# Kernel optimization log

Measured on AMD Instinct MI355X. Metric: run time of the kernel, lower is better.

## Reference

```python
import jax, jax.numpy as jnp
import numpy as np

B, S, D = 2, 2048, 1024
H = 16
DH = D // H  # 64
LN_EPS = 1e-3  # keras LayerNormalization default epsilon


def _layer_norm(x, gamma, beta):
    mu = jnp.mean(x, axis=-1, keepdims=True)
    var = jnp.mean(jnp.square(x - mu), axis=-1, keepdims=True)
    return (x - mu) * jax.lax.rsqrt(var + LN_EPS) * gamma + beta


def setup_inputs() -> dict:
    key = jax.random.key(0)
    ks = jax.random.split(key, 7)
    he = lambda k, fi, fo: jax.random.normal(k, (fi, fo), jnp.float32) * np.sqrt(2.0 / fi)
    return {
        "query": jax.random.normal(ks[0], (B, S, D), jnp.float32),
        "Wq": he(ks[1], D, D),
        "Wk": he(ks[2], D, D),
        "Wv": he(ks[3], D, D),
        "W1": he(ks[4], D, D),
        "W2": he(ks[5], D, D),
        "W3": he(ks[6], D, D),
        "gamma": jnp.ones((D,), jnp.float32),
        "beta": jnp.zeros((D,), jnp.float32),
    }


def reference(query, Wq, Wk, Wv, W1, W2, W3, gamma, beta):
    # self-attention: key = value = query; do_residual = True
    def split_heads(t):  # [B,S,D] -> [B,H,S,DH]
        return t.reshape(B, S, H, DH).transpose(0, 2, 1, 3)

    q = split_heads(query @ Wq)
    k = split_heads(query @ Wk)
    v = split_heads(query @ Wv)

    scores = jnp.einsum("bhqd,bhkd->bhqk", q, k) / np.sqrt(DH).astype(np.float32)
    attn = jax.nn.softmax(scores, axis=-1)
    ctx = jnp.einsum("bhqk,bhkd->bhqd", attn, v)  # [B,H,S,DH]
    ctx = ctx.transpose(0, 2, 1, 3).reshape(B, S, D)

    out = ctx @ W1
    out = out + query  # residual with value (== query)
    residual = _layer_norm(out, gamma, beta)  # shared LayerNorm, first use
    out = jax.nn.relu(residual @ W2)  # dense2 has relu activation
    out = out @ W3
    out = out + residual
    out = _layer_norm(out, gamma, beta)  # SAME LayerNorm params, second use
    return out
```

## Files before the change

kernel.cpp:

```cpp
#include <hip/hip_runtime.h>
#include <stdint.h>

typedef __attribute__((ext_vector_type(8))) __bf16 bf16x8;
typedef __attribute__((ext_vector_type(4))) float f32x4;
typedef __attribute__((ext_vector_type(16))) float f32x16;
typedef __attribute__((ext_vector_type(4))) uint32_t u32x4;

#define DEVINL __device__ __forceinline__

constexpr int Bc = 2, Sc = 2048, Dc = 1024, Hc = 16;
constexpr int MSc = Bc * Sc;
constexpr float LN_EPS_C = 1e-3f;
constexpr float QSCALE = 0.125f * 1.44269504f;

DEVINL void gload16(const void* gsrc, const void* lds_dst) {
  auto g = (const __attribute__((address_space(1))) void*)(uintptr_t)gsrc;
  auto l = (__attribute__((address_space(3))) void*)(uint32_t)(uintptr_t)lds_dst;
  __builtin_amdgcn_global_load_lds(g, l, 16, 0, 0);
}

DEVINL uint32_t pkbits(float lo, float hi) {
  uint16_t a = __builtin_bit_cast(uint16_t, (__bf16)lo);
  uint16_t b = __builtin_bit_cast(uint16_t, (__bf16)hi);
  return (uint32_t)a | ((uint32_t)b << 16);
}

DEVINL void plswap(uint32_t& a, uint32_t& b) {
  asm volatile("v_permlane32_swap_b32 %0, %1" : "+v"(a), "+v"(b));
}

template <int EPI, int BN>
__global__ __launch_bounds__(256) void gemm_bt(const __bf16* __restrict__ A,
                                               const __bf16* __restrict__ Bt,
                                               void* __restrict__ Cout,
                                               int M, int N, int K) {
  __shared__ __bf16 Ash[128 * 64];
  __shared__ __bf16 Bsh[BN * 64];
  constexpr int NF = BN / 32;
  const int t = threadIdx.x;
  const int lane = t & 63;
  const int wid = t >> 6;
  const int nbn = N / BN;
  const int bm = blockIdx.x / nbn, bn = blockIdx.x % nbn;
  const int m0 = bm * 128, n0 = bn * BN;
  const int wm = wid >> 1, wn = wid & 1;

  f32x4 acc[4][NF];
  f32x4 zero = {0.f, 0.f, 0.f, 0.f};
#pragma unroll
  for (int i = 0; i < 4; ++i)
#pragma unroll
    for (int j = 0; j < NF; ++j) acc[i][j] = zero;

  for (int k0 = 0; k0 < K; k0 += 64) {
#pragma unroll
    for (int i = 0; i < 4; ++i) {
      int c = i * 256 + t;
      int row = c >> 3;
      int ch = (c & 7) ^ (row & 7);
      gload16(A + (size_t)(m0 + row) * K + k0 + ch * 8,
              (const char*)Ash + (i * 256 + wid * 64) * 16);
    }
#pragma unroll
    for (int i = 0; i < BN / 32; ++i) {
      int c = i * 256 + t;
      int row = c >> 3;
      int ch = (c & 7) ^ (row & 7);
      gload16(Bt + (size_t)(n0 + row) * K + k0 + ch * 8,
              (const char*)Bsh + (i * 256 + wid * 64) * 16);
    }
    __syncthreads();
#pragma unroll
    for (int kk = 0; kk < 2; ++kk) {
      bf16x8 af[4], bfr[NF];
      const int colb = kk * 64 + (lane >> 4) * 16;
#pragma unroll
      for (int mf = 0; mf < 4; ++mf) {
        int row = wm * 64 + mf * 16 + (lane & 15);
        af[mf] = *(const bf16x8*)((const char*)Ash + row * 128 +
                                  (colb ^ ((row & 7) << 4)));
      }
#pragma unroll
      for (int nf = 0; nf < NF; ++nf) {
        int row = wn * (BN / 2) + nf * 16 + (lane & 15);
        bfr[nf] = *(const bf16x8*)((const char*)Bsh + row * 128 +
                                   (colb ^ ((row & 7) << 4)));
      }
#pragma unroll
      for (int mf = 0; mf < 4; ++mf)
#pragma unroll
        for (int nf = 0; nf < NF; ++nf)
          acc[mf][nf] = __builtin_amdgcn_mfma_f32_16x16x32_bf16(
              af[mf], bfr[nf], acc[mf][nf], 0, 0, 0);
    }
    __syncthreads();
  }
#pragma unroll
  for (int mf = 0; mf < 4; ++mf)
#pragma unroll
    for (int nf = 0; nf < NF; ++nf)
#pragma unroll
      for (int r = 0; r < 4; ++r) {
        int row = m0 + wm * 64 + mf * 16 + (lane >> 4) * 4 + r;
        int col = n0 + wn * (BN / 2) + nf * 16 + (lane & 15);
        float v = acc[mf][nf][r];
        if (EPI == 0)
          ((__bf16*)Cout)[(size_t)row * N + col] = (__bf16)v;
        else if (EPI == 1)
          ((float*)Cout)[(size_t)row * N + col] = v;
        else if (EPI == 2)
          ((__bf16*)Cout)[(size_t)row * N + col] = (__bf16)fmaxf(v, 0.f);
        else {
          if (col < 1024) v *= QSCALE;
          ((__bf16*)Cout)[(size_t)row * N + col] = (__bf16)v;
        }
      }
}

__global__ __launch_bounds__(256) void attn_kernel(const __bf16* __restrict__ QK,
                                                   const __bf16* __restrict__ Vt,
                                                   __bf16* __restrict__ ctx) {
  __shared__ __bf16 Ksh[2][64 * 64];
  __shared__ __bf16 Vsh[2][64 * 64];
  const int t = threadIdx.x, lane = t & 63, wid = t >> 6;
  const int b = blockIdx.z, h = blockIdx.y;
  const int q0w = blockIdx.x * 128 + wid * 32;
  const int ql = lane & 31, hl = lane >> 5;

  const __bf16* Qp = QK;
  const __bf16* Kp = QK + 1024;

  bf16x8 qf[4];
#pragma unroll
  for (int kk = 0; kk < 4; ++kk)
    qf[kk] = *(const bf16x8*)(Qp + (size_t)(b * Sc + q0w + ql) * 2048 + h * 64 +
                              kk * 16 + hl * 8);

  f32x16 oacc[2];
#pragma unroll
  for (int nh = 0; nh < 2; ++nh)
#pragma unroll
    for (int r = 0; r < 16; ++r) oacc[nh][r] = 0.f;
  float l_run = 0.f;

  auto stage = [&](int buf, int kt) {
#pragma unroll
    for (int i = 0; i < 2; ++i) {
      int c = i * 256 + t;
      int row = c >> 3;
      int ch = (c & 7) ^ (row & 7);
      gload16(Kp + (size_t)(b * Sc + kt * 64 + row) * 2048 + h * 64 + ch * 8,
              (const char*)Ksh[buf] + (i * 256 + wid * 64) * 16);
    }
#pragma unroll
    for (int i = 0; i < 2; ++i) {
      int c = i * 256 + t;
      int row = c >> 3;
      int ch = (c & 7) ^ (row & 7);
      gload16(Vt + (size_t)(h * 64 + row) * MSc + b * Sc + kt * 64 + ch * 8,
              (const char*)Vsh[buf] + (i * 256 + wid * 64) * 16);
    }
  };

  stage(0, 0);
  __syncthreads();

  for (int kt = 0; kt < Sc / 64; ++kt) {
    const int cur = kt & 1;
    if (kt + 1 < Sc / 64) stage(cur ^ 1, kt + 1);

    f32x16 sacc[2];
#pragma unroll
    for (int mf = 0; mf < 2; ++mf)
#pragma unroll
      for (int r = 0; r < 16; ++r) sacc[mf][r] = 0.f;
#pragma unroll
    for (int kk = 0; kk < 4; ++kk)
#pragma unroll
      for (int mf = 0; mf < 2; ++mf) {
        int row = mf * 32 + ql;
        bf16x8 kf = *(const bf16x8*)((const char*)Ksh[cur] + row * 128 +
                                     ((kk * 32 + hl * 16) ^ ((row & 7) << 4)));
        sacc[mf] =
            __builtin_amdgcn_mfma_f32_32x32x16_bf16(kf, qf[kk], sacc[mf], 0, 0, 0);
      }

    bf16x8 pb[4];
#pragma unroll
    for (int mf = 0; mf < 2; ++mf) {
      float p[16];
#pragma unroll
      for (int r = 0; r < 16; ++r) {
        p[r] = __builtin_exp2f(sacc[mf][r]);
        l_run += p[r];
      }
#pragma unroll
      for (int g = 0; g < 2; ++g) {
        uint32_t wa = pkbits(p[8 * g + 0], p[8 * g + 1]);
        uint32_t wb = pkbits(p[8 * g + 4], p[8 * g + 5]);
        uint32_t wc = pkbits(p[8 * g + 2], p[8 * g + 3]);
        uint32_t wd = pkbits(p[8 * g + 6], p[8 * g + 7]);
        plswap(wa, wb);
        plswap(wc, wd);
        u32x4 uw;
        uw.x = wa;
        uw.y = wc;
        uw.z = wb;
        uw.w = wd;
        pb[mf * 2 + g] = __builtin_bit_cast(bf16x8, uw);
      }
    }

#pragma unroll
    for (int kt2 = 0; kt2 < 4; ++kt2)
#pragma unroll
      for (int nh = 0; nh < 2; ++nh) {
        int row = nh * 32 + ql;
        bf16x8 vf = *(const bf16x8*)((const char*)Vsh[cur] + row * 128 +
                                     ((kt2 * 32 + hl * 16) ^ ((row & 7) << 4)));
        oacc[nh] =
            __builtin_amdgcn_mfma_f32_32x32x16_bf16(vf, pb[kt2], oacc[nh], 0, 0, 0);
      }
    __syncthreads();
  }

  float l_tot = l_run + __shfl_xor(l_run, 32);
  const float inv_l = 1.f / l_tot;
#pragma unroll
  for (int nh = 0; nh < 2; ++nh)
#pragma unroll
    for (int g = 0; g < 4; ++g) {
      union {
        __bf16 hv[4];
        uint2 u;
      } w;
#pragma unroll
      for (int r = 0; r < 4; ++r)
        w.hv[r] = (__bf16)(oacc[nh][4 * g + r] * inv_l);
      int dh0 = nh * 32 + 8 * g + 4 * hl;
      *(uint2*)(ctx + (size_t)(b * Sc + q0w + ql) * Dc + h * 64 + dh0) = w.u;
    }
}

template <int MODE>
__global__ __launch_bounds__(256) void ln_fused(const float* __restrict__ X,
                                                const float* __restrict__ R,
                                                const float* __restrict__ gamma,
                                                const float* __restrict__ beta,
                                                __bf16* __restrict__ out_bf,
                                                float* __restrict__ out_f) {
  const int row = blockIdx.x;
  const int t = threadIdx.x;
  const f32x4 xv = *(const f32x4*)(X + (size_t)row * Dc + t * 4);
  const f32x4 rv = *(const f32x4*)(R + (size_t)row * Dc + t * 4);
  float x[4];
  float s = 0.f, ss = 0.f;
#pragma unroll
  for (int i = 0; i < 4; ++i) {
    x[i] = xv[i] + rv[i];
    s += x[i];
    ss += x[i] * x[i];
  }
#pragma unroll
  for (int m = 1; m < 64; m <<= 1) {
    s += __shfl_xor(s, m);
    ss += __shfl_xor(ss, m);
  }
  __shared__ float sred[8];
  const int wid = t >> 6, lane = t & 63;
  if (lane == 0) {
    sred[wid * 2] = s;
    sred[wid * 2 + 1] = ss;
  }
  __syncthreads();
  s = sred[0] + sred[2] + sred[4] + sred[6];
  ss = sred[1] + sred[3] + sred[5] + sred[7];
  const float mu = s * (1.f / Dc);
  const float var = ss * (1.f / Dc) - mu * mu;
  const float rstd = rsqrtf(var + LN_EPS_C);
  const f32x4 gv = *(const f32x4*)(gamma + t * 4);
  const f32x4 bv = *(const f32x4*)(beta + t * 4);
#pragma unroll
  for (int i = 0; i < 4; ++i) {
    float y = (x[i] - mu) * rstd * gv[i] + bv[i];
    if (MODE == 0) {
      out_bf[(size_t)row * Dc + t * 4 + i] = (__bf16)y;
      out_f[(size_t)row * Dc + t * 4 + i] = y;
    } else {
      out_f[(size_t)row * Dc + t * 4 + i] = y;
    }
  }
}

__global__ __launch_bounds__(256) void wtrans(const float* __restrict__ w0,
                                              const float* __restrict__ w1,
                                              const float* __restrict__ w2,
                                              const float* __restrict__ w3,
                                              const float* __restrict__ w4,
                                              const float* __restrict__ w5,
                                              __bf16* __restrict__ out) {
  const float* ws[6] = {w0, w1, w2, w3, w4, w5};
  const float* w = ws[blockIdx.z];
  __bf16* o = out + (size_t)blockIdx.z * Dc * Dc;
  __shared__ float tile[32][33];
  const int tx = threadIdx.x, ty = threadIdx.y;
  const int c0 = blockIdx.x * 32, r0 = blockIdx.y * 32;
#pragma unroll
  for (int i = 0; i < 4; ++i)
    tile[ty + i * 8][tx] = w[(size_t)(r0 + ty + i * 8) * Dc + c0 + tx];
  __syncthreads();
#pragma unroll
  for (int i = 0; i < 4; ++i)
    o[(size_t)(c0 + ty + i * 8) * Dc + r0 + tx] = (__bf16)tile[tx][ty + i * 8];
}

__global__ __launch_bounds__(256) void castq(const float* __restrict__ in,
                                             __bf16* __restrict__ out, int n4) {
  int i = blockIdx.x * blockDim.x + threadIdx.x;
  if (i < n4) {
    f32x4 v = *(const f32x4*)(in + (size_t)i * 4);
#pragma unroll
    for (int j = 0; j < 4; ++j) out[(size_t)i * 4 + j] = (__bf16)v[j];
  }
}

extern "C" void kernel_launch(void* const* d_in, const int* in_sizes, int n_in,
                              void* d_out, int out_size, void* d_ws,
                              size_t ws_size, hipStream_t stream) {
  const float* query = (const float*)d_in[0];
  const float* Wq = (const float*)d_in[1];
  const float* Wk = (const float*)d_in[2];
  const float* Wv = (const float*)d_in[3];
  const float* W1 = (const float*)d_in[4];
  const float* W2 = (const float*)d_in[5];
  const float* W3 = (const float*)d_in[6];
  const float* gamma = (const float*)d_in[7];
  const float* beta = (const float*)d_in[8];
  float* out = (float*)d_out;

  char* ws = (char*)d_ws;
  const size_t MB = 1u << 20;
  __bf16* Wt = (__bf16*)(ws);
  __bf16* Xbf = (__bf16*)(ws + 12 * MB);
  __bf16* QKb = (__bf16*)(ws + 20 * MB);
  __bf16* Vt = (__bf16*)(ws + 36 * MB);
  __bf16* Ctx = (__bf16*)(ws + 44 * MB);
  float* T1 = (float*)(ws + 52 * MB);
  __bf16* Rbf = (__bf16*)(ws + 68 * MB);
  float* Rf = (float*)(ws + 76 * MB);
  __bf16* H2 = (__bf16*)(ws + 92 * MB);

  const int WD = Dc * Dc;

  wtrans<<<dim3(32, 32, 6), dim3(32, 8), 0, stream>>>(Wq, Wk, Wv, W1, W2, W3, Wt);
  castq<<<4096, 256, 0, stream>>>(query, Xbf, (MSc * Dc) / 4);
  gemm_bt<3, 128><<<32 * 16, 256, 0, stream>>>(Xbf, Wt, QKb, MSc, 2048, Dc);
  gemm_bt<0, 64><<<8 * 64, 256, 0, stream>>>(Wt + 2 * WD, Xbf, Vt, Dc, MSc, Dc);
  attn_kernel<<<dim3(Sc / 128, Hc, Bc), 256, 0, stream>>>(QKb, Vt, Ctx);
  gemm_bt<1, 64><<<32 * 16, 256, 0, stream>>>(Ctx, Wt + 3 * WD, T1, MSc, Dc, Dc);
  ln_fused<0><<<MSc, 256, 0, stream>>>(T1, query, gamma, beta, Rbf, Rf);
  gemm_bt<2, 64><<<32 * 16, 256, 0, stream>>>(Rbf, Wt + 4 * WD, H2, MSc, Dc, Dc);
  gemm_bt<1, 64><<<32 * 16, 256, 0, stream>>>(H2, Wt + 5 * WD, T1, MSc, Dc, Dc);
  ln_fused<1><<<MSc, 256, 0, stream>>>(T1, Rf, gamma, beta, nullptr, out);
}
```

Before: 286.1 us.

## Split attention over key halves, merge QKV GEMMs, compute row sums via MFMA

Attention now splits the key range into two halves, which doubles the grid. Each half writes fp32 partial outputs and row sums, and a new combine kernel merges them into ctx. Row sums are computed with an extra MFMA against a ones vector instead of scalar adds, bf16 packing uses v_cvt_pk_bf16_f32, and the loop is manually double-buffered. The Q/K and V projection GEMMs are merged into one launch, and the V GEMM uses BN=128. GEMM epilogues become runtime parameters. The cost is extra fp32 partial traffic and one more launch, in exchange for more parallelism and fewer VALU ops in the attention kernel.

```diff
diff --git a/kernel.cpp b/kernel.cpp
--- a/kernel.cpp
+++ b/kernel.cpp
@@ -19,21 +19,20 @@
   __builtin_amdgcn_global_load_lds(g, l, 16, 0, 0);
 }
 
-DEVINL uint32_t pkbits(float lo, float hi) {
-  uint16_t a = __builtin_bit_cast(uint16_t, (__bf16)lo);
-  uint16_t b = __builtin_bit_cast(uint16_t, (__bf16)hi);
-  return (uint32_t)a | ((uint32_t)b << 16);
+DEVINL uint32_t cvtpk(float lo, float hi) {
+  uint32_t r;
+  asm("v_cvt_pk_bf16_f32 %0, %1, %2" : "=v"(r) : "v"(lo), "v"(hi));
+  return r;
 }
 
 DEVINL void plswap(uint32_t& a, uint32_t& b) {
   asm volatile("v_permlane32_swap_b32 %0, %1" : "+v"(a), "+v"(b));
 }
 
-template <int EPI, int BN>
-__global__ __launch_bounds__(256) void gemm_bt(const __bf16* __restrict__ A,
-                                               const __bf16* __restrict__ Bt,
-                                               void* __restrict__ Cout,
-                                               int M, int N, int K) {
+template <int BN>
+DEVINL void gemm_core(const __bf16* __restrict__ A, const __bf16* __restrict__ Bt,
+                      void* __restrict__ Cout, int M, int N, int K, int epi,
+                      int blk) {
   __shared__ __bf16 Ash[128 * 64];
   __shared__ __bf16 Bsh[BN * 64];
   constexpr int NF = BN / 32;
@@ -41,7 +40,7 @@
   const int lane = t & 63;
   const int wid = t >> 6;
   const int nbn = N / BN;
-  const int bm = blockIdx.x / nbn, bn = blockIdx.x % nbn;
+  const int bm = blk / nbn, bn = blk % nbn;
   const int m0 = bm * 128, n0 = bn * BN;
   const int wm = wid >> 1, wn = wid & 1;
 
@@ -104,11 +103,11 @@
         int row = m0 + wm * 64 + mf * 16 + (lane >> 4) * 4 + r;
         int col = n0 + wn * (BN / 2) + nf * 16 + (lane & 15);
         float v = acc[mf][nf][r];
-        if (EPI == 0)
+        if (epi == 0)
           ((__bf16*)Cout)[(size_t)row * N + col] = (__bf16)v;
-        else if (EPI == 1)
+        else if (epi == 1)
           ((float*)Cout)[(size_t)row * N + col] = v;
-        else if (EPI == 2)
+        else if (epi == 2)
           ((__bf16*)Cout)[(size_t)row * N + col] = (__bf16)fmaxf(v, 0.f);
         else {
           if (col < 1024) v *= QSCALE;
@@ -117,13 +116,34 @@
       }
 }
 
-__global__ __launch_bounds__(256) void attn_kernel(const __bf16* __restrict__ QK,
-                                                   const __bf16* __restrict__ Vt,
-                                                   __bf16* __restrict__ ctx) {
+template <int BN>
+__global__ __launch_bounds__(256) void gemm_bt(const __bf16* __restrict__ A,
+                                               const __bf16* __restrict__ Bt,
+                                               void* __restrict__ Cout, int M,
+                                               int N, int K, int epi) {
+  gemm_core<BN>(A, Bt, Cout, M, N, K, epi, blockIdx.x);
+}
+
+__global__ __launch_bounds__(256) void gemm_dual(const __bf16* __restrict__ Xbf,
+                                                 const __bf16* __restrict__ Wqk,
+                                                 const __bf16* __restrict__ Wvt,
+                                                 __bf16* __restrict__ QKb,
+                                                 __bf16* __restrict__ Vt) {
+  if (blockIdx.x < 512)
+    gemm_core<128>(Xbf, Wqk, QKb, MSc, 2048, Dc, 3, blockIdx.x);
+  else
+    gemm_core<128>(Wvt, Xbf, Vt, Dc, MSc, Dc, 0, blockIdx.x - 512);
+}
+
+__global__ __launch_bounds__(256, 4) void attn_kernel(
+    const __bf16* __restrict__ QK, const __bf16* __restrict__ Vt,
+    float* __restrict__ Op0, float* __restrict__ Op1,
+    float* __restrict__ lpart) {
   __shared__ __bf16 Ksh[2][64 * 64];
   __shared__ __bf16 Vsh[2][64 * 64];
   const int t = threadIdx.x, lane = t & 63, wid = t >> 6;
-  const int b = blockIdx.z, h = blockIdx.y;
+  const int h = blockIdx.y;
+  const int b = blockIdx.z >> 1, sp = blockIdx.z & 1;
   const int q0w = blockIdx.x * 128 + wid * 32;
   const int ql = lane & 31, hl = lane >> 5;
 
@@ -136,12 +156,19 @@
     qf[kk] = *(const bf16x8*)(Qp + (size_t)(b * Sc + q0w + ql) * 2048 + h * 64 +
                               kk * 16 + hl * 8);
 
-  f32x16 oacc[2];
-#pragma unroll
-  for (int nh = 0; nh < 2; ++nh)
-#pragma unroll
-    for (int r = 0; r < 16; ++r) oacc[nh][r] = 0.f;
-  float l_run = 0.f;
+  u32x4 uo;
+  uo.x = uo.y = uo.z = uo.w = 0x3F803F80u;
+  const bf16x8 onesf = __builtin_bit_cast(bf16x8, uo);
+
+  f32x16 oacc[2], lacc;
+#pragma unroll
+  for (int r = 0; r < 16; ++r) {
+    oacc[0][r] = 0.f;
+    oacc[1][r] = 0.f;
+    lacc[r] = 0.f;
+  }
+
+  const int kt0 = sp * 16;
 
   auto stage = [&](int buf, int kt) {
 #pragma unroll
@@ -162,12 +189,8 @@
     }
   };
 
-  stage(0, 0);
-  __syncthreads();
-
-  for (int kt = 0; kt < Sc / 64; ++kt) {
-    const int cur = kt & 1;
-    if (kt + 1 < Sc / 64) stage(cur ^ 1, kt + 1);
+  auto body = [&](int kti, int cur) {
+    if (kti + 1 < 16) stage(cur ^ 1, kt0 + kti + 1);
 
     f32x16 sacc[2];
 #pragma unroll
@@ -190,16 +213,13 @@
     for (int mf = 0; mf < 2; ++mf) {
       float p[16];
 #pragma unroll
-      for (int r = 0; r < 16; ++r) {
-        p[r] = __builtin_exp2f(sacc[mf][r]);
-        l_run += p[r];
-      }
+      for (int r = 0; r < 16; ++r) p[r] = __builtin_exp2f(sacc[mf][r]);
 #pragma unroll
       for (int g = 0; g < 2; ++g) {
-        uint32_t wa = pkbits(p[8 * g + 0], p[8 * g + 1]);
-        uint32_t wb = pkbits(p[8 * g + 4], p[8 * g + 5]);
-        uint32_t wc = pkbits(p[8 * g + 2], p[8 * g + 3]);
-        uint32_t wd = pkbits(p[8 * g + 6], p[8 * g + 7]);
+        uint32_t wa = cvtpk(p[8 * g + 0], p[8 * g + 1]);
+        uint32_t wb = cvtpk(p[8 * g + 4], p[8 * g + 5]);
+        uint32_t wc = cvtpk(p[8 * g + 2], p[8 * g + 3]);
+        uint32_t wd = cvtpk(p[8 * g + 6], p[8 * g + 7]);
         plswap(wa, wb);
         plswap(wc, wd);
         u32x4 uw;
@@ -212,7 +232,7 @@
     }
 
 #pragma unroll
-    for (int kt2 = 0; kt2 < 4; ++kt2)
+    for (int kt2 = 0; kt2 < 4; ++kt2) {
 #pragma unroll
       for (int nh = 0; nh < 2; ++nh) {
         int row = nh * 32 + ql;
@@ -221,25 +241,52 @@
         oacc[nh] =
             __builtin_amdgcn_mfma_f32_32x32x16_bf16(vf, pb[kt2], oacc[nh], 0, 0, 0);
       }
+      lacc = __builtin_amdgcn_mfma_f32_32x32x16_bf16(onesf, pb[kt2], lacc, 0, 0, 0);
+    }
     __syncthreads();
-  }
-
-  float l_tot = l_run + __shfl_xor(l_run, 32);
-  const float inv_l = 1.f / l_tot;
+  };
+
+  stage(0, kt0);
+  __syncthreads();
+  for (int kp = 0; kp < 8; ++kp) {
+    body(2 * kp, 0);
+    body(2 * kp + 1, 1);
+  }
+
+  float* Ob = sp ? Op1 : Op0;
+  float* Op = Ob + (size_t)(b * Sc + q0w + ql) * Dc + h * 64;
 #pragma unroll
   for (int nh = 0; nh < 2; ++nh)
 #pragma unroll
     for (int g = 0; g < 4; ++g) {
-      union {
-        __bf16 hv[4];
-        uint2 u;
-      } w;
-#pragma unroll
-      for (int r = 0; r < 4; ++r)
-        w.hv[r] = (__bf16)(oacc[nh][4 * g + r] * inv_l);
-      int dh0 = nh * 32 + 8 * g + 4 * hl;
-      *(uint2*)(ctx + (size_t)(b * Sc + q0w + ql) * Dc + h * 64 + dh0) = w.u;
-    }
+      f32x4 v;
+#pragma unroll
+      for (int r = 0; r < 4; ++r) v[r] = oacc[nh][4 * g + r];
+      *(f32x4*)(Op + nh * 32 + 8 * g + 4 * hl) = v;
+    }
+  if (hl == 0)
+    lpart[((size_t)(sp * Bc + b) * Hc + h) * Sc + q0w + ql] = lacc[0];
+}
+
+__global__ __launch_bounds__(256) void attn_combine(const float* __restrict__ O0,
+                                                    const float* __restrict__ O1,
+                                                    const float* __restrict__ lp,
+                                                    __bf16* __restrict__ ctx) {
+  const int r = blockIdx.x, t = threadIdx.x;
+  const int d0 = t * 4, h = d0 >> 6;
+  const int b = r >> 11, s = r & 2047;
+  const float l0 = lp[((size_t)(0 * Bc + b) * Hc + h) * Sc + s];
+  const float l1 = lp[((size_t)(1 * Bc + b) * Hc + h) * Sc + s];
+  const float inv = 1.f / (l0 + l1);
+  const f32x4 a = *(const f32x4*)(O0 + (size_t)r * Dc + d0);
+  const f32x4 c = *(const f32x4*)(O1 + (size_t)r * Dc + d0);
+  union {
+    __bf16 hv[4];
+    uint2 u;
+  } w;
+#pragma unroll
+  for (int i = 0; i < 4; ++i) w.hv[i] = (__bf16)((a[i] + c[i]) * inv);
+  *(uint2*)(ctx + (size_t)r * Dc + d0) = w.u;
 }
 
 template <int MODE>
@@ -351,15 +398,19 @@
   __bf16* H2 = (__bf16*)(ws + 92 * MB);
 
   const int WD = Dc * Dc;
+  float* Op0 = T1;
+  float* Op1 = Rf;
+  float* lpart = (float*)H2;
 
   wtrans<<<dim3(32, 32, 6), dim3(32, 8), 0, stream>>>(Wq, Wk, Wv, W1, W2, W3, Wt);
   castq<<<4096, 256, 0, stream>>>(query, Xbf, (MSc * Dc) / 4);
-  gemm_bt<3, 128><<<32 * 16, 256, 0, stream>>>(Xbf, Wt, QKb, MSc, 2048, Dc);
-  gemm_bt<0, 64><<<8 * 64, 256, 0, stream>>>(Wt + 2 * WD, Xbf, Vt, Dc, MSc, Dc);
-  attn_kernel<<<dim3(Sc / 128, Hc, Bc), 256, 0, stream>>>(QKb, Vt, Ctx);
-  gemm_bt<1, 64><<<32 * 16, 256, 0, stream>>>(Ctx, Wt + 3 * WD, T1, MSc, Dc, Dc);
+  gemm_dual<<<768, 256, 0, stream>>>(Xbf, Wt, Wt + 2 * WD, QKb, Vt);
+  attn_kernel<<<dim3(Sc / 128, Hc, Bc * 2), 256, 0, stream>>>(QKb, Vt, Op0, Op1,
+                                                              lpart);
+  attn_combine<<<MSc, 256, 0, stream>>>(Op0, Op1, lpart, Ctx);
+  gemm_bt<64><<<32 * 16, 256, 0, stream>>>(Ctx, Wt + 3 * WD, T1, MSc, Dc, Dc, 1);
   ln_fused<0><<<MSc, 256, 0, stream>>>(T1, query, gamma, beta, Rbf, Rf);
-  gemm_bt<2, 64><<<32 * 16, 256, 0, stream>>>(Rbf, Wt + 4 * WD, H2, MSc, Dc, Dc);
-  gemm_bt<1, 64><<<32 * 16, 256, 0, stream>>>(H2, Wt + 5 * WD, T1, MSc, Dc, Dc);
+  gemm_bt<64><<<32 * 16, 256, 0, stream>>>(Rbf, Wt + 4 * WD, H2, MSc, Dc, Dc, 2);
+  gemm_bt<64><<<32 * 16, 256, 0, stream>>>(H2, Wt + 5 * WD, T1, MSc, Dc, Dc, 1);
   ln_fused<1><<<MSc, 256, 0, stream>>>(T1, Rf, gamma, beta, nullptr, out);
 }
```

After: 307.7 us. 1.08x slower.

## Split-K the W1/W3 GEMMs, deepen attention buffering, remap attention grid

Applied to the files above, without the earlier changes.

Adds a split-K-by-2 GEMM that writes two fp32 partial outputs, which the LayerNorm kernel now sums together with the residual. This doubles the block count for the W1 and W3 projections to improve occupancy. The attention kernel moves to a four-buffer K/V pipeline with half as many barriers, a flattened grid that interleaves batch-heads, a packed bf16 convert instruction, and split running sums. The cost is extra fp32 partial traffic and more LDS per attention block.

```diff
diff --git a/kernel.cpp b/kernel.cpp
--- a/kernel.cpp
+++ b/kernel.cpp
@@ -19,10 +19,10 @@
   __builtin_amdgcn_global_load_lds(g, l, 16, 0, 0);
 }
 
-DEVINL uint32_t pkbits(float lo, float hi) {
-  uint16_t a = __builtin_bit_cast(uint16_t, (__bf16)lo);
-  uint16_t b = __builtin_bit_cast(uint16_t, (__bf16)hi);
-  return (uint32_t)a | ((uint32_t)b << 16);
+DEVINL uint32_t cvtpk(float lo, float hi) {
+  uint32_t r;
+  asm("v_cvt_pk_bf16_f32 %0, %1, %2" : "=v"(r) : "v"(lo), "v"(hi));
+  return r;
 }
 
 DEVINL void plswap(uint32_t& a, uint32_t& b) {
@@ -117,14 +117,105 @@
       }
 }
 
+template <int BN>
+__global__ __launch_bounds__(256) void gemm_bt_sk2(const __bf16* __restrict__ A,
+                                                   const __bf16* __restrict__ Bt,
+                                                   float* __restrict__ C0,
+                                                   float* __restrict__ C1,
+                                                   int M, int N, int K) {
+  __shared__ __bf16 Ash[128 * 64];
+  __shared__ __bf16 Bsh[BN * 64];
+  constexpr int NF = BN / 32;
+  const int t = threadIdx.x;
+  const int lane = t & 63;
+  const int wid = t >> 6;
+  const int nbn = N / BN;
+  const int nb = (M / 128) * nbn;
+  int blk = blockIdx.x;
+  int ks = 0;
+  float* Cout = C0;
+  if (blk >= nb) {
+    blk -= nb;
+    ks = K / 2;
+    Cout = C1;
+  }
+  const int bm = blk / nbn, bn = blk % nbn;
+  const int m0 = bm * 128, n0 = bn * BN;
+  const int wm = wid >> 1, wn = wid & 1;
+
+  f32x4 acc[4][NF];
+  f32x4 zero = {0.f, 0.f, 0.f, 0.f};
+#pragma unroll
+  for (int i = 0; i < 4; ++i)
+#pragma unroll
+    for (int j = 0; j < NF; ++j) acc[i][j] = zero;
+
+  for (int k0 = ks; k0 < ks + K / 2; k0 += 64) {
+#pragma unroll
+    for (int i = 0; i < 4; ++i) {
+      int c = i * 256 + t;
+      int row = c >> 3;
+      int ch = (c & 7) ^ (row & 7);
+      gload16(A + (size_t)(m0 + row) * K + k0 + ch * 8,
+              (const char*)Ash + (i * 256 + wid * 64) * 16);
+    }
+#pragma unroll
+    for (int i = 0; i < BN / 32; ++i) {
+      int c = i * 256 + t;
+      int row = c >> 3;
+      int ch = (c & 7) ^ (row & 7);
+      gload16(Bt + (size_t)(n0 + row) * K + k0 + ch * 8,
+              (const char*)Bsh + (i * 256 + wid * 64) * 16);
+    }
+    __syncthreads();
+#pragma unroll
+    for (int kk = 0; kk < 2; ++kk) {
+      bf16x8 af[4], bfr[NF];
+      const int colb = kk * 64 + (lane >> 4) * 16;
+#pragma unroll
+      for (int mf = 0; mf < 4; ++mf) {
+        int row = wm * 64 + mf * 16 + (lane & 15);
+        af[mf] = *(const bf16x8*)((const char*)Ash + row * 128 +
+                                  (colb ^ ((row & 7) << 4)));
+      }
+#pragma unroll
+      for (int nf = 0; nf < NF; ++nf) {
+        int row = wn * (BN / 2) + nf * 16 + (lane & 15);
+        bfr[nf] = *(const bf16x8*)((const char*)Bsh + row * 128 +
+                                   (colb ^ ((row & 7) << 4)));
+      }
+#pragma unroll
+      for (int mf = 0; mf < 4; ++mf)
+#pragma unroll
+        for (int nf = 0; nf < NF; ++nf)
+          acc[mf][nf] = __builtin_amdgcn_mfma_f32_16x16x32_bf16(
+              af[mf], bfr[nf], acc[mf][nf], 0, 0, 0);
+    }
+    __syncthreads();
+  }
+#pragma unroll
+  for (int mf = 0; mf < 4; ++mf)
+#pragma unroll
+    for (int nf = 0; nf < NF; ++nf)
+#pragma unroll
+      for (int r = 0; r < 4; ++r) {
+        int row = m0 + wm * 64 + mf * 16 + (lane >> 4) * 4 + r;
+        int col = n0 + wn * (BN / 2) + nf * 16 + (lane & 15);
+        Cout[(size_t)row * N + col] = acc[mf][nf][r];
+      }
+}
+
 __global__ __launch_bounds__(256) void attn_kernel(const __bf16* __restrict__ QK,
                                                    const __bf16* __restrict__ Vt,
                                                    __bf16* __restrict__ ctx) {
-  __shared__ __bf16 Ksh[2][64 * 64];
-  __shared__ __bf16 Vsh[2][64 * 64];
+  __shared__ __bf16 Ksh[4][64 * 64];
+  __shared__ __bf16 Vsh[4][64 * 64];
   const int t = threadIdx.x, lane = t & 63, wid = t >> 6;
-  const int b = blockIdx.z, h = blockIdx.y;
-  const int q0w = blockIdx.x * 128 + wid * 32;
+  const int flat = blockIdx.x;
+  const int bh = (flat & 7) * 4 + ((flat >> 3) & 3);
+  const int qt = flat >> 5;
+  const int b = bh >> 4, h = bh & 15;
+  const int q0w = qt * 128 + wid * 32;
   const int ql = lane & 31, hl = lane >> 5;
 
   const __bf16* Qp = QK;
@@ -138,10 +229,11 @@
 
   f32x16 oacc[2];
 #pragma unroll
-  for (int nh = 0; nh < 2; ++nh)
-#pragma unroll
-    for (int r = 0; r < 16; ++r) oacc[nh][r] = 0.f;
-  float l_run = 0.f;
+  for (int r = 0; r < 16; ++r) {
+    oacc[0][r] = 0.f;
+    oacc[1][r] = 0.f;
+  }
+  float l0 = 0.f, l1 = 0.f;
 
   auto stage = [&](int buf, int kt) {
 #pragma unroll
@@ -162,13 +254,7 @@
     }
   };
 
-  stage(0, 0);
-  __syncthreads();
-
-  for (int kt = 0; kt < Sc / 64; ++kt) {
-    const int cur = kt & 1;
-    if (kt + 1 < Sc / 64) stage(cur ^ 1, kt + 1);
-
+  auto body = [&](int buf) {
     f32x16 sacc[2];
 #pragma unroll
     for (int mf = 0; mf < 2; ++mf)
@@ -179,7 +265,7 @@
 #pragma unroll
       for (int mf = 0; mf < 2; ++mf) {
         int row = mf * 32 + ql;
-        bf16x8 kf = *(const bf16x8*)((const char*)Ksh[cur] + row * 128 +
+        bf16x8 kf = *(const bf16x8*)((const char*)Ksh[buf] + row * 128 +
                                      ((kk * 32 + hl * 16) ^ ((row & 7) << 4)));
         sacc[mf] =
             __builtin_amdgcn_mfma_f32_32x32x16_bf16(kf, qf[kk], sacc[mf], 0, 0, 0);
@@ -192,14 +278,17 @@
 #pragma unroll
       for (int r = 0; r < 16; ++r) {
         p[r] = __builtin_exp2f(sacc[mf][r]);
-        l_run += p[r];
+        if (r & 1)
+          l1 += p[r];
+        else
+          l0 += p[r];
       }
 #pragma unroll
       for (int g = 0; g < 2; ++g) {
-        uint32_t wa = pkbits(p[8 * g + 0], p[8 * g + 1]);
-        uint32_t wb = pkbits(p[8 * g + 4], p[8 * g + 5]);
-        uint32_t wc = pkbits(p[8 * g + 2], p[8 * g + 3]);
-        uint32_t wd = pkbits(p[8 * g + 6], p[8 * g + 7]);
+        uint32_t wa = cvtpk(p[8 * g + 0], p[8 * g + 1]);
+        uint32_t wb = cvtpk(p[8 * g + 4], p[8 * g + 5]);
+        uint32_t wc = cvtpk(p[8 * g + 2], p[8 * g + 3]);
+        uint32_t wd = cvtpk(p[8 * g + 6], p[8 * g + 7]);
         plswap(wa, wb);
         plswap(wc, wd);
         u32x4 uw;
@@ -216,15 +305,34 @@
 #pragma unroll
       for (int nh = 0; nh < 2; ++nh) {
         int row = nh * 32 + ql;
-        bf16x8 vf = *(const bf16x8*)((const char*)Vsh[cur] + row * 128 +
+        bf16x8 vf = *(const bf16x8*)((const char*)Vsh[buf] + row * 128 +
                                      ((kt2 * 32 + hl * 16) ^ ((row & 7) << 4)));
         oacc[nh] =
             __builtin_amdgcn_mfma_f32_32x32x16_bf16(vf, pb[kt2], oacc[nh], 0, 0, 0);
       }
-    __syncthreads();
-  }
-
-  float l_tot = l_run + __shfl_xor(l_run, 32);
+  };
+
+  stage(0, 0);
+  stage(1, 1);
+  __syncthreads();
+  for (int q = 0; q < 8; ++q) {
+    const int t0 = 4 * q;
+    stage(2, t0 + 2);
+    stage(3, t0 + 3);
+    body(0);
+    body(1);
+    __syncthreads();
+    if (t0 + 4 < 32) {
+      stage(0, t0 + 4);
+      stage(1, t0 + 5);
+    }
+    body(2);
+    body(3);
+    __syncthreads();
+  }
+
+  const float l_run = l0 + l1;
+  const float l_tot = l_run + __shfl_xor(l_run, 32);
   const float inv_l = 1.f / l_tot;
 #pragma unroll
   for (int nh = 0; nh < 2; ++nh)
@@ -243,7 +351,8 @@
 }
 
 template <int MODE>
-__global__ __launch_bounds__(256) void ln_fused(const float* __restrict__ X,
+__global__ __launch_bounds__(256) void ln_fused(const float* __restrict__ X0,
+                                                const float* __restrict__ X1,
                                                 const float* __restrict__ R,
                                                 const float* __restrict__ gamma,
                                                 const float* __restrict__ beta,
@@ -251,13 +360,14 @@
                                                 float* __restrict__ out_f) {
   const int row = blockIdx.x;
   const int t = threadIdx.x;
-  const f32x4 xv = *(const f32x4*)(X + (size_t)row * Dc + t * 4);
+  const f32x4 xv0 = *(const f32x4*)(X0 + (size_t)row * Dc + t * 4);
+  const f32x4 xv1 = *(const f32x4*)(X1 + (size_t)row * Dc + t * 4);
   const f32x4 rv = *(const f32x4*)(R + (size_t)row * Dc + t * 4);
   float x[4];
   float s = 0.f, ss = 0.f;
 #pragma unroll
   for (int i = 0; i < 4; ++i) {
-    x[i] = xv[i] + rv[i];
+    x[i] = xv0[i] + xv1[i] + rv[i];
     s += x[i];
     ss += x[i] * x[i];
   }
@@ -345,10 +455,11 @@
   __bf16* QKb = (__bf16*)(ws + 20 * MB);
   __bf16* Vt = (__bf16*)(ws + 36 * MB);
   __bf16* Ctx = (__bf16*)(ws + 44 * MB);
-  float* T1 = (float*)(ws + 52 * MB);
+  float* Ta = (float*)(ws + 52 * MB);
   __bf16* Rbf = (__bf16*)(ws + 68 * MB);
   float* Rf = (float*)(ws + 76 * MB);
   __bf16* H2 = (__bf16*)(ws + 92 * MB);
+  float* Tb = (float*)(ws + 20 * MB);
 
   const int WD = Dc * Dc;
 
@@ -356,10 +467,12 @@
   castq<<<4096, 256, 0, stream>>>(query, Xbf, (MSc * Dc) / 4);
   gemm_bt<3, 128><<<32 * 16, 256, 0, stream>>>(Xbf, Wt, QKb, MSc, 2048, Dc);
   gemm_bt<0, 64><<<8 * 64, 256, 0, stream>>>(Wt + 2 * WD, Xbf, Vt, Dc, MSc, Dc);
-  attn_kernel<<<dim3(Sc / 128, Hc, Bc), 256, 0, stream>>>(QKb, Vt, Ctx);
-  gemm_bt<1, 64><<<32 * 16, 256, 0, stream>>>(Ctx, Wt + 3 * WD, T1, MSc, Dc, Dc);
-  ln_fused<0><<<MSc, 256, 0, stream>>>(T1, query, gamma, beta, Rbf, Rf);
+  attn_kernel<<<512, 256, 0, stream>>>(QKb, Vt, Ctx);
+  gemm_bt_sk2<64><<<2 * 32 * 16, 256, 0, stream>>>(Ctx, Wt + 3 * WD, Ta, Tb,
+                                                   MSc, Dc, Dc);
+  ln_fused<0><<<MSc, 256, 0, stream>>>(Ta, Tb, query, gamma, beta, Rbf, Rf);
   gemm_bt<2, 64><<<32 * 16, 256, 0, stream>>>(Rbf, Wt + 4 * WD, H2, MSc, Dc, Dc);
-  gemm_bt<1, 64><<<32 * 16, 256, 0, stream>>>(H2, Wt + 5 * WD, T1, MSc, Dc, Dc);
-  ln_fused<1><<<MSc, 256, 0, stream>>>(T1, Rf, gamma, beta, nullptr, out);
-}
+  gemm_bt_sk2<64><<<2 * 32 * 16, 256, 0, stream>>>(H2, Wt + 5 * WD, Ta, Tb,
+                                                   MSc, Dc, Dc);
+  ln_fused<1><<<MSc, 256, 0, stream>>>(Ta, Tb, Rf, gamma, beta, nullptr, out);
+}
```

After: 300.5 us. 5.0% more time.

## Double-buffer GEMM LDS, enlarge attention blocks, use packed bf16 convert

Applied to the files above, without the earlier changes.

The GEMM kernel gets double-buffered LDS tiles so the next K slice loads while the current one computes, with one barrier per iteration instead of two. The attention kernel moves to 512-thread blocks covering 256 queries, launched on a flat grid with remapped batch/head order, and each thread stages one K and one V chunk. Softmax row sums are split across four accumulators, and bf16 packing uses v_cvt_pk_bf16_f32 inline asm, with volatile dropped from the permlane asm. The QK projection GEMM switches to BN=64 with twice as many blocks. Together these raise LDS use per block and change occupancy and scheduling freedom, with a more complex kernel in exchange.

```diff
diff --git a/kernel.cpp b/kernel.cpp
--- a/kernel.cpp
+++ b/kernel.cpp
@@ -19,14 +19,14 @@
   __builtin_amdgcn_global_load_lds(g, l, 16, 0, 0);
 }
 
-DEVINL uint32_t pkbits(float lo, float hi) {
-  uint16_t a = __builtin_bit_cast(uint16_t, (__bf16)lo);
-  uint16_t b = __builtin_bit_cast(uint16_t, (__bf16)hi);
-  return (uint32_t)a | ((uint32_t)b << 16);
+DEVINL uint32_t cvtpk(float lo, float hi) {
+  uint32_t r;
+  asm("v_cvt_pk_bf16_f32 %0, %1, %2" : "=v"(r) : "v"(lo), "v"(hi));
+  return r;
 }
 
 DEVINL void plswap(uint32_t& a, uint32_t& b) {
-  asm volatile("v_permlane32_swap_b32 %0, %1" : "+v"(a), "+v"(b));
+  asm("v_permlane32_swap_b32 %0, %1" : "+v"(a), "+v"(b));
 }
 
 template <int EPI, int BN>
@@ -34,8 +34,8 @@
                                                const __bf16* __restrict__ Bt,
                                                void* __restrict__ Cout,
                                                int M, int N, int K) {
-  __shared__ __bf16 Ash[128 * 64];
-  __shared__ __bf16 Bsh[BN * 64];
+  __shared__ __bf16 Ash[2][128 * 64];
+  __shared__ __bf16 Bsh[2][BN * 64];
   constexpr int NF = BN / 32;
   const int t = threadIdx.x;
   const int lane = t & 63;
@@ -52,14 +52,14 @@
 #pragma unroll
     for (int j = 0; j < NF; ++j) acc[i][j] = zero;
 
-  for (int k0 = 0; k0 < K; k0 += 64) {
+  auto stage = [&](int buf, int k0) {
 #pragma unroll
     for (int i = 0; i < 4; ++i) {
       int c = i * 256 + t;
       int row = c >> 3;
       int ch = (c & 7) ^ (row & 7);
       gload16(A + (size_t)(m0 + row) * K + k0 + ch * 8,
-              (const char*)Ash + (i * 256 + wid * 64) * 16);
+              (const char*)Ash[buf] + (i * 256 + wid * 64) * 16);
     }
 #pragma unroll
     for (int i = 0; i < BN / 32; ++i) {
@@ -67,9 +67,15 @@
       int row = c >> 3;
       int ch = (c & 7) ^ (row & 7);
       gload16(Bt + (size_t)(n0 + row) * K + k0 + ch * 8,
-              (const char*)Bsh + (i * 256 + wid * 64) * 16);
-    }
-    __syncthreads();
+              (const char*)Bsh[buf] + (i * 256 + wid * 64) * 16);
+    }
+  };
+
+  stage(0, 0);
+  __syncthreads();
+  for (int k0 = 0; k0 < K; k0 += 64) {
+    const int buf = (k0 >> 6) & 1;
+    if (k0 + 64 < K) stage(buf ^ 1, k0 + 64);
 #pragma unroll
     for (int kk = 0; kk < 2; ++kk) {
       bf16x8 af[4], bfr[NF];
@@ -77,13 +83,13 @@
 #pragma unroll
       for (int mf = 0; mf < 4; ++mf) {
         int row = wm * 64 + mf * 16 + (lane & 15);
-        af[mf] = *(const bf16x8*)((const char*)Ash + row * 128 +
+        af[mf] = *(const bf16x8*)((const char*)Ash[buf] + row * 128 +
                                   (colb ^ ((row & 7) << 4)));
       }
 #pragma unroll
       for (int nf = 0; nf < NF; ++nf) {
         int row = wn * (BN / 2) + nf * 16 + (lane & 15);
-        bfr[nf] = *(const bf16x8*)((const char*)Bsh + row * 128 +
+        bfr[nf] = *(const bf16x8*)((const char*)Bsh[buf] + row * 128 +
                                    (colb ^ ((row & 7) << 4)));
       }
 #pragma unroll
@@ -117,14 +123,17 @@
       }
 }
 
-__global__ __launch_bounds__(256) void attn_kernel(const __bf16* __restrict__ QK,
-                                                   const __bf16* __restrict__ Vt,
-                                                   __bf16* __restrict__ ctx) {
+__global__ __launch_bounds__(512, 4) void attn_kernel(const __bf16* __restrict__ QK,
+                                                      const __bf16* __restrict__ Vt,
+                                                      __bf16* __restrict__ ctx) {
   __shared__ __bf16 Ksh[2][64 * 64];
   __shared__ __bf16 Vsh[2][64 * 64];
   const int t = threadIdx.x, lane = t & 63, wid = t >> 6;
-  const int b = blockIdx.z, h = blockIdx.y;
-  const int q0w = blockIdx.x * 128 + wid * 32;
+  const int flat = blockIdx.x;
+  const int bh = (flat & 7) * 4 + ((flat >> 3) & 3);
+  const int qt = flat >> 5;
+  const int b = bh >> 4, h = bh & 15;
+  const int q0w = qt * 256 + wid * 32;
   const int ql = lane & 31, hl = lane >> 5;
 
   const __bf16* Qp = QK;
@@ -138,37 +147,22 @@
 
   f32x16 oacc[2];
 #pragma unroll
-  for (int nh = 0; nh < 2; ++nh)
-#pragma unroll
-    for (int r = 0; r < 16; ++r) oacc[nh][r] = 0.f;
-  float l_run = 0.f;
+  for (int r = 0; r < 16; ++r) {
+    oacc[0][r] = 0.f;
+    oacc[1][r] = 0.f;
+  }
+  float l0 = 0.f, l1 = 0.f, l2 = 0.f, l3 = 0.f;
 
   auto stage = [&](int buf, int kt) {
-#pragma unroll
-    for (int i = 0; i < 2; ++i) {
-      int c = i * 256 + t;
-      int row = c >> 3;
-      int ch = (c & 7) ^ (row & 7);
-      gload16(Kp + (size_t)(b * Sc + kt * 64 + row) * 2048 + h * 64 + ch * 8,
-              (const char*)Ksh[buf] + (i * 256 + wid * 64) * 16);
-    }
-#pragma unroll
-    for (int i = 0; i < 2; ++i) {
-      int c = i * 256 + t;
-      int row = c >> 3;
-      int ch = (c & 7) ^ (row & 7);
-      gload16(Vt + (size_t)(h * 64 + row) * MSc + b * Sc + kt * 64 + ch * 8,
-              (const char*)Vsh[buf] + (i * 256 + wid * 64) * 16);
-    }
+    const int row = t >> 3;
+    const int ch = (t & 7) ^ (row & 7);
+    gload16(Kp + (size_t)(b * Sc + kt * 64 + row) * 2048 + h * 64 + ch * 8,
+            (const char*)Ksh[buf] + wid * 1024);
+    gload16(Vt + (size_t)(h * 64 + row) * MSc + b * Sc + kt * 64 + ch * 8,
+            (const char*)Vsh[buf] + wid * 1024);
   };
 
-  stage(0, 0);
-  __syncthreads();
-
-  for (int kt = 0; kt < Sc / 64; ++kt) {
-    const int cur = kt & 1;
-    if (kt + 1 < Sc / 64) stage(cur ^ 1, kt + 1);
-
+  auto body = [&](int buf) {
     f32x16 sacc[2];
 #pragma unroll
     for (int mf = 0; mf < 2; ++mf)
@@ -179,7 +173,7 @@
 #pragma unroll
       for (int mf = 0; mf < 2; ++mf) {
         int row = mf * 32 + ql;
-        bf16x8 kf = *(const bf16x8*)((const char*)Ksh[cur] + row * 128 +
+        bf16x8 kf = *(const bf16x8*)((const char*)Ksh[buf] + row * 128 +
                                      ((kk * 32 + hl * 16) ^ ((row & 7) << 4)));
         sacc[mf] =
             __builtin_amdgcn_mfma_f32_32x32x16_bf16(kf, qf[kk], sacc[mf], 0, 0, 0);
@@ -192,14 +186,21 @@
 #pragma unroll
       for (int r = 0; r < 16; ++r) {
         p[r] = __builtin_exp2f(sacc[mf][r]);
-        l_run += p[r];
+        if ((r & 3) == 0)
+          l0 += p[r];
+        else if ((r & 3) == 1)
+          l1 += p[r];
+        else if ((r & 3) == 2)
+          l2 += p[r];
+        else
+          l3 += p[r];
       }
 #pragma unroll
       for (int g = 0; g < 2; ++g) {
-        uint32_t wa = pkbits(p[8 * g + 0], p[8 * g + 1]);
-        uint32_t wb = pkbits(p[8 * g + 4], p[8 * g + 5]);
-        uint32_t wc = pkbits(p[8 * g + 2], p[8 * g + 3]);
-        uint32_t wd = pkbits(p[8 * g + 6], p[8 * g + 7]);
+        uint32_t wa = cvtpk(p[8 * g + 0], p[8 * g + 1]);
+        uint32_t wb = cvtpk(p[8 * g + 4], p[8 * g + 5]);
+        uint32_t wc = cvtpk(p[8 * g + 2], p[8 * g + 3]);
+        uint32_t wd = cvtpk(p[8 * g + 6], p[8 * g + 7]);
         plswap(wa, wb);
         plswap(wc, wd);
         u32x4 uw;
@@ -216,15 +217,24 @@
 #pragma unroll
       for (int nh = 0; nh < 2; ++nh) {
         int row = nh * 32 + ql;
-        bf16x8 vf = *(const bf16x8*)((const char*)Vsh[cur] + row * 128 +
+        bf16x8 vf = *(const bf16x8*)((const char*)Vsh[buf] + row * 128 +
                                      ((kt2 * 32 + hl * 16) ^ ((row & 7) << 4)));
         oacc[nh] =
             __builtin_amdgcn_mfma_f32_32x32x16_bf16(vf, pb[kt2], oacc[nh], 0, 0, 0);
       }
+  };
+
+  stage(0, 0);
+  __syncthreads();
+  for (int kt = 0; kt < Sc / 64; ++kt) {
+    const int buf = kt & 1;
+    if (kt + 1 < Sc / 64) stage(buf ^ 1, kt + 1);
+    body(buf);
     __syncthreads();
   }
 
-  float l_tot = l_run + __shfl_xor(l_run, 32);
+  const float l_run = (l0 + l1) + (l2 + l3);
+  const float l_tot = l_run + __shfl_xor(l_run, 32);
   const float inv_l = 1.f / l_tot;
 #pragma unroll
   for (int nh = 0; nh < 2; ++nh)
@@ -354,9 +364,9 @@
 
   wtrans<<<dim3(32, 32, 6), dim3(32, 8), 0, stream>>>(Wq, Wk, Wv, W1, W2, W3, Wt);
   castq<<<4096, 256, 0, stream>>>(query, Xbf, (MSc * Dc) / 4);
-  gemm_bt<3, 128><<<32 * 16, 256, 0, stream>>>(Xbf, Wt, QKb, MSc, 2048, Dc);
+  gemm_bt<3, 64><<<32 * 32, 256, 0, stream>>>(Xbf, Wt, QKb, MSc, 2048, Dc);
   gemm_bt<0, 64><<<8 * 64, 256, 0, stream>>>(Wt + 2 * WD, Xbf, Vt, Dc, MSc, Dc);
-  attn_kernel<<<dim3(Sc / 128, Hc, Bc), 256, 0, stream>>>(QKb, Vt, Ctx);
+  attn_kernel<<<256, 512, 0, stream>>>(QKb, Vt, Ctx);
   gemm_bt<1, 64><<<32 * 16, 256, 0, stream>>>(Ctx, Wt + 3 * WD, T1, MSc, Dc, Dc);
   ln_fused<0><<<MSc, 256, 0, stream>>>(T1, query, gamma, beta, Rbf, Rf);
   gemm_bt<2, 64><<<32 * 16, 256, 0, stream>>>(Rbf, Wt + 4 * WD, H2, MSc, Dc, Dc);
```

After: 260.5 us. -8.9%, faster.
